# Performance work log

Hardware: AMD Instinct MI355X
Metric: run time of the kernel (lower is better)

## Reference

```python
import jax, jax.numpy as jnp
import numpy as np

N_NODES = 100000
N_EDGES = 1600000
NUM_FEATURES = 256
HIDDEN_DIM = 128
NUM_CLASSES = 16


def setup_inputs() -> dict:
    key = jax.random.key(0)
    k1, k2, k3, k4 = jax.random.split(key, 4)
    x = jax.random.normal(k1, (N_NODES, NUM_FEATURES), dtype=jnp.float32)
    edge_index = jax.random.randint(k2, (2, N_EDGES), 0, N_NODES, dtype=jnp.int64)
    # Glorot-style init like PyG GCNConv's Linear
    W1 = jax.random.normal(k3, (NUM_FEATURES, HIDDEN_DIM), dtype=jnp.float32) / np.sqrt(NUM_FEATURES)
    b1 = jnp.zeros((HIDDEN_DIM,), dtype=jnp.float32)
    W2 = jax.random.normal(k4, (HIDDEN_DIM, NUM_CLASSES), dtype=jnp.float32) / np.sqrt(HIDDEN_DIM)
    b2 = jnp.zeros((NUM_CLASSES,), dtype=jnp.float32)
    return {"x": x, "edge_index": edge_index, "W1": W1, "b1": b1, "W2": W2, "b2": b2}


def _gcn_norm(edge_index, num_nodes):
    """PyG GCNConv default: add self-loops, symmetric deg^{-1/2} A deg^{-1/2} norm."""
    loops = jnp.arange(num_nodes, dtype=edge_index.dtype)
    row = jnp.concatenate([edge_index[0], loops])  # source
    col = jnp.concatenate([edge_index[1], loops])  # target
    deg = jax.ops.segment_sum(jnp.ones_like(col, dtype=jnp.float32), col,
                              num_segments=num_nodes)
    dinv = jnp.where(deg > 0, jax.lax.rsqrt(deg), 0.0)
    norm = dinv[row] * dinv[col]  # [E + N]
    return row, col, norm


def _gcn_conv(h, row, col, norm, num_nodes):
    # transform first (PyG: lin then propagate), then normalized sum-aggregate
    msg = h[row] * norm[:, None]            # [E+N, d] gather + scale
    return jax.ops.segment_sum(msg, col, num_segments=num_nodes)


def reference(x, edge_index, W1, b1, W2, b2):
    num_nodes = x.shape[0]
    row, col, norm = _gcn_norm(edge_index, num_nodes)
    h = x @ W1
    h = _gcn_conv(h, row, col, norm, num_nodes) + b1
    h = jax.nn.relu(h)
    h = h @ W2
    out = _gcn_conv(h, row, col, norm, num_nodes) + b2
    return out
```

## Files before the change

kernel.cpp:

```cpp
#include <hip/hip_runtime.h>

#define N_NODES 100000
#define N_EDGES 1600000
#define F_IN    256
#define F_HID   128
#define F_OUT   16

#define BSHIFT  9
#define BNODES  512
#define NB      196
#define CHUNK   4096
#define NCHUNK  ((N_EDGES + CHUNK - 1) / CHUNK)

typedef __attribute__((ext_vector_type(8))) short short8;
typedef __attribute__((ext_vector_type(4))) float float4v;

__device__ __forceinline__ unsigned int bf16_rn(float f) {
    unsigned int u = __float_as_uint(f);
    return (u + 0x7FFFu + ((u >> 16) & 1u)) >> 16;
}
__device__ __forceinline__ unsigned int pk2(float lo, float hi) {
    return bf16_rn(lo) | (bf16_rn(hi) << 16);
}
__device__ __forceinline__ float blo(unsigned int u) { return __uint_as_float(u << 16); }
__device__ __forceinline__ float bhi(unsigned int u) { return __uint_as_float(u & 0xFFFF0000u); }


__global__ __launch_bounds__(256) void k_bhist(const int* __restrict__ coli,
                                               int* __restrict__ bcnt) {
    __shared__ int lc[NB];
    int tid = threadIdx.x;
    for (int i = tid; i < NB; i += 256) lc[i] = 0;
    __syncthreads();
    for (int e = blockIdx.x * 256 + tid; e < N_EDGES; e += 256 * 256)
        atomicAdd(&lc[coli[e] >> BSHIFT], 1);
    __syncthreads();
    for (int i = tid; i < NB; i += 256)
        if (lc[i]) atomicAdd(&bcnt[i], lc[i]);
}

__global__ __launch_bounds__(256) void k_bscan(const int* __restrict__ bcnt,
                                               int* __restrict__ bbase,
                                               int* __restrict__ bcur) {
    __shared__ int sc[256];
    int t = threadIdx.x;
    int v = (t < NB) ? bcnt[t] : 0;
    sc[t] = v; __syncthreads();
    for (int off = 1; off < 256; off <<= 1) {
        int x = (t >= off) ? sc[t - off] : 0;
        __syncthreads();
        sc[t] += x;
        __syncthreads();
    }
    if (t < NB) {
        int e = sc[t] - v;
        bbase[t] = e;
        bcur[t]  = e;
    }
    if (t == 0) bbase[NB] = N_EDGES;
}

__global__ __launch_bounds__(256) void k_binscatter(const int* __restrict__ rowi,
                                                    const int* __restrict__ coli,
                                                    int* __restrict__ bcur,
                                                    unsigned int* __restrict__ ebuf) {
    __shared__ int cnt[NB], gbase[NB], run[NB];
    int tid = threadIdx.x;
    int e0 = blockIdx.x * CHUNK;
    for (int i = tid; i < NB; i += 256) { cnt[i] = 0; run[i] = 0; }
    __syncthreads();
    int d[16], s[16];
    #pragma unroll
    for (int i = 0; i < 16; i++) {
        int e = e0 + i * 256 + tid;
        if (e < N_EDGES) {
            d[i] = coli[e]; s[i] = rowi[e];
            atomicAdd(&cnt[d[i] >> BSHIFT], 1);
        } else d[i] = -1;
    }
    __syncthreads();
    for (int i = tid; i < NB; i += 256)
        gbase[i] = cnt[i] ? atomicAdd(&bcur[i], cnt[i]) : 0;
    __syncthreads();
    #pragma unroll
    for (int i = 0; i < 16; i++) {
        if (d[i] >= 0) {
            int b = d[i] >> BSHIFT;
            int off = atomicAdd(&run[b], 1);
            ebuf[gbase[b] + off] = ((unsigned int)(d[i] & 511) << 17) | (unsigned int)s[i];
        }
    }
}

__global__ __launch_bounds__(256) void k_finalize(const int* __restrict__ bbase,
                                                  const unsigned int* __restrict__ ebuf,
                                                  int* __restrict__ row_ptr,
                                                  float* __restrict__ dinv,
                                                  int* __restrict__ esrc) {
    __shared__ int ndeg[BNODES];
    __shared__ int sc[BNODES];
    int tid = threadIdx.x;
    int b   = blockIdx.x;
    int nb0 = b << BSHIFT;
    int ebeg = bbase[b], eend = bbase[b + 1];
    ndeg[tid] = 0; ndeg[tid + 256] = 0;
    __syncthreads();
    for (int e = ebeg + tid; e < eend; e += 256)
        atomicAdd(&ndeg[ebuf[e] >> 17], 1);
    __syncthreads();
    int i0 = tid, i1 = tid + 256;
    sc[i0] = ndeg[i0]; sc[i1] = ndeg[i1];
    __syncthreads();
    for (int off = 1; off < BNODES; off <<= 1) {
        int v0 = (i0 >= off) ? sc[i0 - off] : 0;
        int v1 = (i1 >= off) ? sc[i1 - off] : 0;
        __syncthreads();
        sc[i0] += v0; sc[i1] += v1;
        __syncthreads();
    }
    #pragma unroll
    for (int k = 0; k < 2; k++) {
        int i = tid + k * 256;
        int n = nb0 + i;
        int deg = ndeg[i];
        int excl = sc[i] - deg;
        if (n < N_NODES) {
            row_ptr[n] = ebeg + excl;
            dinv[n]    = rsqrtf(1.0f + (float)deg);
        }
        ndeg[i] = excl;
    }
    if (b == NB - 1 && tid == 0) row_ptr[N_NODES] = N_EDGES;
    __syncthreads();
    for (int e = ebeg + tid; e < eend; e += 256) {
        unsigned int p = ebuf[e];
        int off = atomicAdd(&ndeg[p >> 17], 1);
        esrc[ebeg + off] = (int)(p & 0x1FFFFu);
    }
}


__global__ __launch_bounds__(256) void k_transW(const float* __restrict__ W1,
                                                ushort* __restrict__ Wt) {
    int t = blockIdx.x * 256 + threadIdx.x;
    int c = t & 127, k = t >> 7;
    Wt[c * 256 + k] = (ushort)bf16_rn(W1[k * 128 + c]);
}


__global__ __launch_bounds__(256) void k_gemm1(const float* __restrict__ x,
                                               const ushort* __restrict__ Wt,
                                               const float* __restrict__ dinv,
                                               ushort* __restrict__ g1) {
    __shared__ ushort Bl[128 * 256];
    const int tid = threadIdx.x;
    const int w = tid >> 6;
    const int l = tid & 63;
    const int m = l & 15;
    const int q = l >> 4;
    const int R0 = blockIdx.x * 128;

    {
        const uint4* Wg = (const uint4*)Wt;
        uint4* Bl4 = (uint4*)Bl;
        #pragma unroll
        for (int it = 0; it < 16; it++) {
            int i = it * 256 + tid;
            int c = i >> 5, j = i & 31;
            Bl4[c * 32 + (j ^ (c & 7))] = Wg[i];
        }
    }
    __syncthreads();

    int r0 = R0 + w * 32 + m;      if (r0 > N_NODES - 1) r0 = N_NODES - 1;
    int r1 = R0 + w * 32 + 16 + m; if (r1 > N_NODES - 1) r1 = N_NODES - 1;
    const float* xr0 = &x[(size_t)r0 * F_IN + q * 8];
    const float* xr1 = &x[(size_t)r1 * F_IN + q * 8];
    const short8* Bl8 = (const short8*)Bl;

    float4v acc[2][8];
    #pragma unroll
    for (int i = 0; i < 2; i++)
        #pragma unroll
        for (int j = 0; j < 8; j++) acc[i][j] = (float4v){0.f, 0.f, 0.f, 0.f};

    #pragma unroll 2
    for (int kt = 0; kt < F_IN; kt += 32) {
        float4 a0 = *(const float4*)&xr0[kt];
        float4 a1 = *(const float4*)&xr0[kt + 4];
        float4 b0 = *(const float4*)&xr1[kt];
        float4 b1 = *(const float4*)&xr1[kt + 4];
        short8 af0, af1;
        ((uint*)&af0)[0] = pk2(a0.x, a0.y); ((uint*)&af0)[1] = pk2(a0.z, a0.w);
        ((uint*)&af0)[2] = pk2(a1.x, a1.y); ((uint*)&af0)[3] = pk2(a1.z, a1.w);
        ((uint*)&af1)[0] = pk2(b0.x, b0.y); ((uint*)&af1)[1] = pk2(b0.z, b0.w);
        ((uint*)&af1)[2] = pk2(b1.x, b1.y); ((uint*)&af1)[3] = pk2(b1.z, b1.w);
        int jq = (kt >> 3) + q;
        #pragma unroll
        for (int n = 0; n < 8; n++) {
            int col = n * 16 + m;
            short8 bfr = Bl8[col * 32 + (jq ^ (col & 7))];
            acc[0][n] = __builtin_amdgcn_mfma_f32_16x16x32_bf16(af0, bfr, acc[0][n], 0, 0, 0);
            acc[1][n] = __builtin_amdgcn_mfma_f32_16x16x32_bf16(af1, bfr, acc[1][n], 0, 0, 0);
        }
    }

    const int rbase = R0 + w * 32 + q * 4;
    float dv0[4], dv1[4];
    #pragma unroll
    for (int r = 0; r < 4; r++) {
        int v0 = rbase + r;      dv0[r] = (v0 < N_NODES) ? dinv[v0] : 0.f;
        int v1 = rbase + 16 + r; dv1[r] = (v1 < N_NODES) ? dinv[v1] : 0.f;
    }
    #pragma unroll
    for (int n = 0; n < 8; n++) {
        #pragma unroll
        for (int r = 0; r < 4; r++) {
            int v0 = rbase + r;
            if (v0 < N_NODES)
                g1[v0 * F_HID + n * 16 + m] = (ushort)bf16_rn(dv0[r] * acc[0][n][r]);
            int v1 = rbase + 16 + r;
            if (v1 < N_NODES)
                g1[v1 * F_HID + n * 16 + m] = (ushort)bf16_rn(dv1[r] * acc[1][n][r]);
        }
    }
}


__global__ __launch_bounds__(256) void k_agg1g2(const int* __restrict__ row_ptr,
                                                const int* __restrict__ esrc,
                                                const float* __restrict__ dinv,
                                                const unsigned int* __restrict__ g1,
                                                const float* __restrict__ b1,
                                                const float* __restrict__ W2,
                                                float* __restrict__ g2) {
    __shared__ float hl[4][132];
    __shared__ float W2s[F_HID * F_OUT];
    const int tid  = threadIdx.x;
    const int wave = tid >> 6;
    const int lane = tid & 63;
    const int node = blockIdx.x * 4 + wave;

    for (int i = tid; i < F_HID * F_OUT; i += 256) W2s[i] = W2[i];
    __syncthreads();

    int s = row_ptr[node], t = row_ptr[node + 1];
    unsigned int u = g1[node * 64 + lane];
    float ax = blo(u), ay = bhi(u);
    int e = s;
    for (; e + 7 < t; e += 8) {
        int r0 = esrc[e],     r1 = esrc[e + 1], r2 = esrc[e + 2], r3 = esrc[e + 3];
        int r4 = esrc[e + 4], r5 = esrc[e + 5], r6 = esrc[e + 6], r7 = esrc[e + 7];
        unsigned int u0 = g1[r0 * 64 + lane], u1 = g1[r1 * 64 + lane];
        unsigned int u2 = g1[r2 * 64 + lane], u3 = g1[r3 * 64 + lane];
        unsigned int u4 = g1[r4 * 64 + lane], u5 = g1[r5 * 64 + lane];
        unsigned int u6 = g1[r6 * 64 + lane], u7 = g1[r7 * 64 + lane];
        ax += blo(u0) + blo(u1) + blo(u2) + blo(u3)
            + blo(u4) + blo(u5) + blo(u6) + blo(u7);
        ay += bhi(u0) + bhi(u1) + bhi(u2) + bhi(u3)
            + bhi(u4) + bhi(u5) + bhi(u6) + bhi(u7);
    }
    for (; e + 3 < t; e += 4) {
        int r0 = esrc[e], r1 = esrc[e + 1], r2 = esrc[e + 2], r3 = esrc[e + 3];
        unsigned int u0 = g1[r0 * 64 + lane], u1 = g1[r1 * 64 + lane];
        unsigned int u2 = g1[r2 * 64 + lane], u3 = g1[r3 * 64 + lane];
        ax += blo(u0) + blo(u1) + blo(u2) + blo(u3);
        ay += bhi(u0) + bhi(u1) + bhi(u2) + bhi(u3);
    }
    for (; e < t; e++) {
        unsigned int u0 = g1[esrc[e] * 64 + lane];
        ax += blo(u0); ay += bhi(u0);
    }
    float wv = dinv[node];
    float2 bb = ((const float2*)b1)[lane];
    hl[wave][lane * 2]     = fmaxf(fmaf(wv, ax, bb.x), 0.0f);
    hl[wave][lane * 2 + 1] = fmaxf(fmaf(wv, ay, bb.y), 0.0f);

    const int col = lane & 15, part = lane >> 4;
    float acc = 0.f;
    #pragma unroll
    for (int i = 0; i < 32; i++) {
        int f = i * 4 + part;
        acc = fmaf(hl[wave][f], W2s[f * 16 + col], acc);
    }
    acc += __shfl_xor(acc, 16);
    acc += __shfl_xor(acc, 32);
    if (lane < 16) g2[node * 16 + col] = wv * acc;
}


__global__ __launch_bounds__(256) void k_agg2(const int* __restrict__ row_ptr,
                                              const int* __restrict__ esrc,
                                              const float* __restrict__ dinv,
                                              const float* __restrict__ g2,
                                              const float* __restrict__ b2,
                                              float* __restrict__ out) {
    int gid = blockIdx.x * 256 + threadIdx.x;
    int node = gid >> 4;
    int f = gid & 15;
    if (node >= N_NODES) return;
    int s = row_ptr[node], t = row_ptr[node + 1];
    float acc = g2[node * 16 + f];
    int e = s;
    for (; e + 7 < t; e += 8) {
        float a0 = g2[esrc[e] * 16 + f],     a1 = g2[esrc[e + 1] * 16 + f];
        float a2 = g2[esrc[e + 2] * 16 + f], a3 = g2[esrc[e + 3] * 16 + f];
        float a4 = g2[esrc[e + 4] * 16 + f], a5 = g2[esrc[e + 5] * 16 + f];
        float a6 = g2[esrc[e + 6] * 16 + f], a7 = g2[esrc[e + 7] * 16 + f];
        acc += a0 + a1 + a2 + a3 + a4 + a5 + a6 + a7;
    }
    for (; e + 3 < t; e += 4) {
        acc += g2[esrc[e] * 16 + f] + g2[esrc[e + 1] * 16 + f]
             + g2[esrc[e + 2] * 16 + f] + g2[esrc[e + 3] * 16 + f];
    }
    for (; e < t; e++) acc += g2[esrc[e] * 16 + f];
    out[node * 16 + f] = fmaf(dinv[node], acc, b2[f]);
}


extern "C" void kernel_launch(void* const* d_in, const int* in_sizes, int n_in,
                              void* d_out, int out_size, void* d_ws, size_t ws_size,
                              hipStream_t stream) {
    const float* x   = (const float*)d_in[0];
    const int*   ei  = (const int*)d_in[1];
    const float* W1  = (const float*)d_in[2];
    const float* b1  = (const float*)d_in[3];
    const float* W2  = (const float*)d_in[4];
    const float* b2  = (const float*)d_in[5];
    float* out = (float*)d_out;

    const int* rowi = ei;
    const int* coli = ei + N_EDGES;

    char* ws = (char*)d_ws;
    int*          bcnt    = (int*)(ws + 0);
    int*          bbase   = (int*)(ws + 4096);
    int*          bcur    = (int*)(ws + 8192);
    int*          row_ptr = (int*)(ws + 16384);
    float*        dinv    = (float*)(ws + 524288);
    unsigned int* ebuf    = (unsigned int*)(ws + 1048576);
    int*          esrc    = (int*)(ws + 8388608);
    ushort*       Wt      = (ushort*)(ws + 15728640);
    ushort*       g1      = (ushort*)(ws + 16777216);
    float*        g2      = (float*)(ws + 45088768);

    hipMemsetAsync(bcnt, 0, NB * sizeof(int), stream);

    k_bhist     <<<256, 256, 0, stream>>>(coli, bcnt);
    k_bscan     <<<1, 256, 0, stream>>>(bcnt, bbase, bcur);
    k_binscatter<<<NCHUNK, 256, 0, stream>>>(rowi, coli, bcur, ebuf);
    k_finalize  <<<NB, 256, 0, stream>>>(bbase, ebuf, row_ptr, dinv, esrc);
    k_transW    <<<128, 256, 0, stream>>>(W1, Wt);

    k_gemm1     <<<(N_NODES + 127) / 128, 256, 0, stream>>>(x, Wt, dinv, g1);
    k_agg1g2    <<<N_NODES / 4, 256, 0, stream>>>(row_ptr, esrc, dinv,
                                                  (const unsigned int*)g1, b1, W2, g2);
    k_agg2      <<<(N_NODES * 16 + 255) / 256, 256, 0, stream>>>(row_ptr, esrc, dinv, g2, b2, out);
}
```

Measured before the change: 358.7 us.

## Use fixed-capacity bins, bf16 layer-2 features, and register-held W2 with multi-node waves

```diff
diff --git a/kernel.cpp b/kernel.cpp
--- a/kernel.cpp
+++ b/kernel.cpp
@@ -9,6 +9,7 @@
 #define BSHIFT  9
 #define BNODES  512
 #define NB      196
+#define ECAP    16384
 #define CHUNK   4096
 #define NCHUNK  ((N_EDGES + CHUNK - 1) / CHUNK)
 
@@ -24,40 +25,12 @@
 }
 __device__ __forceinline__ float blo(unsigned int u) { return __uint_as_float(u << 16); }
 __device__ __forceinline__ float bhi(unsigned int u) { return __uint_as_float(u & 0xFFFF0000u); }
-
-
-__global__ __launch_bounds__(256) void k_bhist(const int* __restrict__ coli,
-                                               int* __restrict__ bcnt) {
-    __shared__ int lc[NB];
-    int tid = threadIdx.x;
-    for (int i = tid; i < NB; i += 256) lc[i] = 0;
-    __syncthreads();
-    for (int e = blockIdx.x * 256 + tid; e < N_EDGES; e += 256 * 256)
-        atomicAdd(&lc[coli[e] >> BSHIFT], 1);
-    __syncthreads();
-    for (int i = tid; i < NB; i += 256)
-        if (lc[i]) atomicAdd(&bcnt[i], lc[i]);
-}
-
-__global__ __launch_bounds__(256) void k_bscan(const int* __restrict__ bcnt,
-                                               int* __restrict__ bbase,
-                                               int* __restrict__ bcur) {
-    __shared__ int sc[256];
-    int t = threadIdx.x;
-    int v = (t < NB) ? bcnt[t] : 0;
-    sc[t] = v; __syncthreads();
-    for (int off = 1; off < 256; off <<= 1) {
-        int x = (t >= off) ? sc[t - off] : 0;
-        __syncthreads();
-        sc[t] += x;
-        __syncthreads();
-    }
-    if (t < NB) {
-        int e = sc[t] - v;
-        bbase[t] = e;
-        bcur[t]  = e;
-    }
-    if (t == 0) bbase[NB] = N_EDGES;
+__device__ __forceinline__ float bfu(unsigned short u) { return __uint_as_float(((unsigned int)u) << 16); }
+
+
+__global__ __launch_bounds__(256) void k_binit(int* __restrict__ bcur) {
+    int i = threadIdx.x;
+    if (i < NB) bcur[i] = i * ECAP;
 }
 
 __global__ __launch_bounds__(256) void k_binscatter(const int* __restrict__ rowi,
@@ -92,9 +65,10 @@
     }
 }
 
-__global__ __launch_bounds__(256) void k_finalize(const int* __restrict__ bbase,
+__global__ __launch_bounds__(256) void k_finalize(const int* __restrict__ bcur,
                                                   const unsigned int* __restrict__ ebuf,
-                                                  int* __restrict__ row_ptr,
+                                                  int* __restrict__ rp_start,
+                                                  int* __restrict__ rp_end,
                                                   float* __restrict__ dinv,
                                                   int* __restrict__ esrc) {
     __shared__ int ndeg[BNODES];
@@ -102,7 +76,7 @@
     int tid = threadIdx.x;
     int b   = blockIdx.x;
     int nb0 = b << BSHIFT;
-    int ebeg = bbase[b], eend = bbase[b + 1];
+    int ebeg = b * ECAP, eend = bcur[b];
     ndeg[tid] = 0; ndeg[tid + 256] = 0;
     __syncthreads();
     for (int e = ebeg + tid; e < eend; e += 256)
@@ -125,12 +99,12 @@
         int deg = ndeg[i];
         int excl = sc[i] - deg;
         if (n < N_NODES) {
-            row_ptr[n] = ebeg + excl;
-            dinv[n]    = rsqrtf(1.0f + (float)deg);
+            rp_start[n] = ebeg + excl;
+            rp_end[n]   = ebeg + excl + deg;
+            dinv[n]     = rsqrtf(1.0f + (float)deg);
         }
         ndeg[i] = excl;
     }
-    if (b == NB - 1 && tid == 0) row_ptr[N_NODES] = N_EDGES;
     __syncthreads();
     for (int e = ebeg + tid; e < eend; e += 256) {
         unsigned int p = ebuf[e];
@@ -227,93 +201,97 @@
 }
 
 
-__global__ __launch_bounds__(256) void k_agg1g2(const int* __restrict__ row_ptr,
+__global__ __launch_bounds__(256) void k_agg1g2(const int* __restrict__ rp_start,
+                                                const int* __restrict__ rp_end,
                                                 const int* __restrict__ esrc,
                                                 const float* __restrict__ dinv,
                                                 const unsigned int* __restrict__ g1,
                                                 const float* __restrict__ b1,
                                                 const float* __restrict__ W2,
-                                                float* __restrict__ g2) {
+                                                ushort* __restrict__ g2b) {
     __shared__ float hl[4][132];
-    __shared__ float W2s[F_HID * F_OUT];
     const int tid  = threadIdx.x;
     const int wave = tid >> 6;
     const int lane = tid & 63;
-    const int node = blockIdx.x * 4 + wave;
-
-    for (int i = tid; i < F_HID * F_OUT; i += 256) W2s[i] = W2[i];
-    __syncthreads();
-
-    int s = row_ptr[node], t = row_ptr[node + 1];
-    unsigned int u = g1[node * 64 + lane];
-    float ax = blo(u), ay = bhi(u);
-    int e = s;
-    for (; e + 7 < t; e += 8) {
-        int r0 = esrc[e],     r1 = esrc[e + 1], r2 = esrc[e + 2], r3 = esrc[e + 3];
-        int r4 = esrc[e + 4], r5 = esrc[e + 5], r6 = esrc[e + 6], r7 = esrc[e + 7];
-        unsigned int u0 = g1[r0 * 64 + lane], u1 = g1[r1 * 64 + lane];
-        unsigned int u2 = g1[r2 * 64 + lane], u3 = g1[r3 * 64 + lane];
-        unsigned int u4 = g1[r4 * 64 + lane], u5 = g1[r5 * 64 + lane];
-        unsigned int u6 = g1[r6 * 64 + lane], u7 = g1[r7 * 64 + lane];
-        ax += blo(u0) + blo(u1) + blo(u2) + blo(u3)
-            + blo(u4) + blo(u5) + blo(u6) + blo(u7);
-        ay += bhi(u0) + bhi(u1) + bhi(u2) + bhi(u3)
-            + bhi(u4) + bhi(u5) + bhi(u6) + bhi(u7);
-    }
-    for (; e + 3 < t; e += 4) {
-        int r0 = esrc[e], r1 = esrc[e + 1], r2 = esrc[e + 2], r3 = esrc[e + 3];
-        unsigned int u0 = g1[r0 * 64 + lane], u1 = g1[r1 * 64 + lane];
-        unsigned int u2 = g1[r2 * 64 + lane], u3 = g1[r3 * 64 + lane];
-        ax += blo(u0) + blo(u1) + blo(u2) + blo(u3);
-        ay += bhi(u0) + bhi(u1) + bhi(u2) + bhi(u3);
-    }
-    for (; e < t; e++) {
-        unsigned int u0 = g1[esrc[e] * 64 + lane];
-        ax += blo(u0); ay += bhi(u0);
-    }
-    float wv = dinv[node];
+    const int col  = lane & 15, part = lane >> 4;
+
+    float w2r[32];
+    #pragma unroll
+    for (int i = 0; i < 32; i++) w2r[i] = W2[i * 64 + lane];
+
     float2 bb = ((const float2*)b1)[lane];
-    hl[wave][lane * 2]     = fmaxf(fmaf(wv, ax, bb.x), 0.0f);
-    hl[wave][lane * 2 + 1] = fmaxf(fmaf(wv, ay, bb.y), 0.0f);
-
-    const int col = lane & 15, part = lane >> 4;
-    float acc = 0.f;
-    #pragma unroll
-    for (int i = 0; i < 32; i++) {
-        int f = i * 4 + part;
-        acc = fmaf(hl[wave][f], W2s[f * 16 + col], acc);
-    }
-    acc += __shfl_xor(acc, 16);
-    acc += __shfl_xor(acc, 32);
-    if (lane < 16) g2[node * 16 + col] = wv * acc;
-}
-
-
-__global__ __launch_bounds__(256) void k_agg2(const int* __restrict__ row_ptr,
+
+    #pragma unroll 1
+    for (int j = 0; j < 4; j++) {
+        const int node = blockIdx.x * 16 + j * 4 + wave;
+        int s = rp_start[node], t = rp_end[node];
+        unsigned int u = g1[node * 64 + lane];
+        float ax = blo(u), ay = bhi(u);
+        int e = s;
+        for (; e + 7 < t; e += 8) {
+            int r0 = esrc[e],     r1 = esrc[e + 1], r2 = esrc[e + 2], r3 = esrc[e + 3];
+            int r4 = esrc[e + 4], r5 = esrc[e + 5], r6 = esrc[e + 6], r7 = esrc[e + 7];
+            unsigned int u0 = g1[r0 * 64 + lane], u1 = g1[r1 * 64 + lane];
+            unsigned int u2 = g1[r2 * 64 + lane], u3 = g1[r3 * 64 + lane];
+            unsigned int u4 = g1[r4 * 64 + lane], u5 = g1[r5 * 64 + lane];
+            unsigned int u6 = g1[r6 * 64 + lane], u7 = g1[r7 * 64 + lane];
+            ax += blo(u0) + blo(u1) + blo(u2) + blo(u3)
+                + blo(u4) + blo(u5) + blo(u6) + blo(u7);
+            ay += bhi(u0) + bhi(u1) + bhi(u2) + bhi(u3)
+                + bhi(u4) + bhi(u5) + bhi(u6) + bhi(u7);
+        }
+        for (; e + 3 < t; e += 4) {
+            int r0 = esrc[e], r1 = esrc[e + 1], r2 = esrc[e + 2], r3 = esrc[e + 3];
+            unsigned int u0 = g1[r0 * 64 + lane], u1 = g1[r1 * 64 + lane];
+            unsigned int u2 = g1[r2 * 64 + lane], u3 = g1[r3 * 64 + lane];
+            ax += blo(u0) + blo(u1) + blo(u2) + blo(u3);
+            ay += bhi(u0) + bhi(u1) + bhi(u2) + bhi(u3);
+        }
+        for (; e < t; e++) {
+            unsigned int u0 = g1[esrc[e] * 64 + lane];
+            ax += blo(u0); ay += bhi(u0);
+        }
+        float wv = dinv[node];
+        hl[wave][lane * 2]     = fmaxf(fmaf(wv, ax, bb.x), 0.0f);
+        hl[wave][lane * 2 + 1] = fmaxf(fmaf(wv, ay, bb.y), 0.0f);
+
+        float acc = 0.f;
+        #pragma unroll
+        for (int i = 0; i < 32; i++)
+            acc = fmaf(hl[wave][i * 4 + part], w2r[i], acc);
+        acc += __shfl_xor(acc, 16);
+        acc += __shfl_xor(acc, 32);
+        if (lane < 16) g2b[node * 16 + col] = (ushort)bf16_rn(wv * acc);
+    }
+}
+
+
+__global__ __launch_bounds__(256) void k_agg2(const int* __restrict__ rp_start,
+                                              const int* __restrict__ rp_end,
                                               const int* __restrict__ esrc,
                                               const float* __restrict__ dinv,
-                                              const float* __restrict__ g2,
+                                              const ushort* __restrict__ g2b,
                                               const float* __restrict__ b2,
                                               float* __restrict__ out) {
     int gid = blockIdx.x * 256 + threadIdx.x;
     int node = gid >> 4;
     int f = gid & 15;
     if (node >= N_NODES) return;
-    int s = row_ptr[node], t = row_ptr[node + 1];
-    float acc = g2[node * 16 + f];
+    int s = rp_start[node], t = rp_end[node];
+    float acc = bfu(g2b[node * 16 + f]);
     int e = s;
     for (; e + 7 < t; e += 8) {
-        float a0 = g2[esrc[e] * 16 + f],     a1 = g2[esrc[e + 1] * 16 + f];
-        float a2 = g2[esrc[e + 2] * 16 + f], a3 = g2[esrc[e + 3] * 16 + f];
-        float a4 = g2[esrc[e + 4] * 16 + f], a5 = g2[esrc[e + 5] * 16 + f];
-        float a6 = g2[esrc[e + 6] * 16 + f], a7 = g2[esrc[e + 7] * 16 + f];
+        float a0 = bfu(g2b[esrc[e] * 16 + f]),     a1 = bfu(g2b[esrc[e + 1] * 16 + f]);
+        float a2 = bfu(g2b[esrc[e + 2] * 16 + f]), a3 = bfu(g2b[esrc[e + 3] * 16 + f]);
+        float a4 = bfu(g2b[esrc[e + 4] * 16 + f]), a5 = bfu(g2b[esrc[e + 5] * 16 + f]);
+        float a6 = bfu(g2b[esrc[e + 6] * 16 + f]), a7 = bfu(g2b[esrc[e + 7] * 16 + f]);
         acc += a0 + a1 + a2 + a3 + a4 + a5 + a6 + a7;
     }
     for (; e + 3 < t; e += 4) {
-        acc += g2[esrc[e] * 16 + f] + g2[esrc[e + 1] * 16 + f]
-             + g2[esrc[e + 2] * 16 + f] + g2[esrc[e + 3] * 16 + f];
-    }
-    for (; e < t; e++) acc += g2[esrc[e] * 16 + f];
+        acc += bfu(g2b[esrc[e] * 16 + f]) + bfu(g2b[esrc[e + 1] * 16 + f])
+             + bfu(g2b[esrc[e + 2] * 16 + f]) + bfu(g2b[esrc[e + 3] * 16 + f]);
+    }
+    for (; e < t; e++) acc += bfu(g2b[esrc[e] * 16 + f]);
     out[node * 16 + f] = fmaf(dinv[node], acc, b2[f]);
 }
 
@@ -333,27 +311,24 @@
     const int* coli = ei + N_EDGES;
 
     char* ws = (char*)d_ws;
-    int*          bcnt    = (int*)(ws + 0);
-    int*          bbase   = (int*)(ws + 4096);
-    int*          bcur    = (int*)(ws + 8192);
-    int*          row_ptr = (int*)(ws + 16384);
-    float*        dinv    = (float*)(ws + 524288);
-    unsigned int* ebuf    = (unsigned int*)(ws + 1048576);
-    int*          esrc    = (int*)(ws + 8388608);
-    ushort*       Wt      = (ushort*)(ws + 15728640);
-    ushort*       g1      = (ushort*)(ws + 16777216);
-    float*        g2      = (float*)(ws + 45088768);
-
-    hipMemsetAsync(bcnt, 0, NB * sizeof(int), stream);
-
-    k_bhist     <<<256, 256, 0, stream>>>(coli, bcnt);
-    k_bscan     <<<1, 256, 0, stream>>>(bcnt, bbase, bcur);
+    int*          bcur     = (int*)(ws + 0);
+    int*          rp_start = (int*)(ws + 8192);
+    int*          rp_end   = (int*)(ws + 524288);
+    float*        dinv     = (float*)(ws + 1048576);
+    unsigned int* ebuf     = (unsigned int*)(ws + 2097152);
+    int*          esrc     = (int*)(ws + 16777216);
+    ushort*       Wt       = (ushort*)(ws + 31457280);
+    ushort*       g1       = (ushort*)(ws + 33554432);
+    ushort*       g2b      = (ushort*)(ws + 62914560);
+
+    k_binit     <<<1, 256, 0, stream>>>(bcur);
     k_binscatter<<<NCHUNK, 256, 0, stream>>>(rowi, coli, bcur, ebuf);
-    k_finalize  <<<NB, 256, 0, stream>>>(bbase, ebuf, row_ptr, dinv, esrc);
+    k_finalize  <<<NB, 256, 0, stream>>>(bcur, ebuf, rp_start, rp_end, dinv, esrc);
     k_transW    <<<128, 256, 0, stream>>>(W1, Wt);
 
     k_gemm1     <<<(N_NODES + 127) / 128, 256, 0, stream>>>(x, Wt, dinv, g1);
-    k_agg1g2    <<<N_NODES / 4, 256, 0, stream>>>(row_ptr, esrc, dinv,
-                                                  (const unsigned int*)g1, b1, W2, g2);
-    k_agg2      <<<(N_NODES * 16 + 255) / 256, 256, 0, stream>>>(row_ptr, esrc, dinv, g2, b2, out);
-}
+    k_agg1g2    <<<N_NODES / 16, 256, 0, stream>>>(rp_start, rp_end, esrc, dinv,
+                                                   (const unsigned int*)g1, b1, W2, g2b);
+    k_agg2      <<<(N_NODES * 16 + 255) / 256, 256, 0, stream>>>(rp_start, rp_end, esrc,
+                                                                 dinv, g2b, b2, out);
+}
```

Measured after the change: 328.3 us. -8.5%, faster.
